# Performance work log

Hardware: AMD Instinct MI355X
Metric: run time of the kernel (lower is better)

## Reference

```python
import jax, jax.numpy as jnp
import numpy as np


def setup_inputs() -> dict:
    key = jax.random.key(0)
    k1, k2, k3, k4 = jax.random.split(key, 4)
    T, E, H, I = 256, 16, 2048, 1024
    x = jax.random.normal(k1, (T, H), dtype=jnp.float32)
    router_logits = jax.random.normal(k2, (T, E), dtype=jnp.float32)
    # dequantized GGUF expert weights (math after dequant is plain fp GEMM)
    w1 = jax.random.normal(k3, (E, 2 * I, H), dtype=jnp.float32) * 0.02  # gate/up fused
    w2 = jax.random.normal(k4, (E, H, I), dtype=jnp.float32) * 0.02     # down proj
    return {"x": x, "router_logits": router_logits, "w1": w1, "w2": w2, "top_k": 4}


def reference(x, router_logits, w1, w2, top_k):
    # Router: softmax -> top-k -> renormalize (vLLM fused_moe default)
    probs = jax.nn.softmax(router_logits, axis=-1)            # [T, E]
    topk_vals, topk_idx = jax.lax.top_k(probs, top_k)          # [T, k]
    topk_vals = topk_vals / jnp.sum(topk_vals, axis=-1, keepdims=True)
    T, E = router_logits.shape
    # dense routing weights (zero for non-selected experts)
    route_w = jnp.zeros((T, E), dtype=x.dtype).at[
        jnp.arange(T)[:, None], topk_idx].set(topk_vals)       # [T, E]

    I = w1.shape[1] // 2
    # gate_up projection for all experts: [T, E, 2I]
    h = jnp.einsum('th,eih->tei', x, w1)
    gate, up = h[..., :I], h[..., I:]
    act = jax.nn.silu(gate) * up                               # silu_and_mul [T, E, I]
    # down projection: [T, E, H]
    y = jnp.einsum('tei,ehi->teh', act, w2)
    # combine with routing weights
    out = jnp.einsum('te,teh->th', route_w, y)                 # [T, H]
    return out
```

## Files before the change

kernel.cpp:

```cpp
#include <hip/hip_runtime.h>


typedef __attribute__((ext_vector_type(8))) short bf16x8;
typedef __attribute__((ext_vector_type(4))) float floatx4;

#define T_TOK 256
#define N_EXP 16
#define H_DIM 2048
#define I_DIM 1024
#define MAX_SLOTS 256

__device__ __forceinline__ short f2bf(float f) {
    union { float f; unsigned u; } v; v.f = f;
    unsigned r = (v.u + 0x7FFFu + ((v.u >> 16) & 1u)) >> 16;
    return (short)r;
}
__device__ __forceinline__ float bf2f(short s) {
    union { unsigned u; float f; } v; v.u = ((unsigned)(unsigned short)s) << 16;
    return v.f;
}
__device__ __forceinline__ bf16x8 pack8(const float* __restrict__ p) {
    float4 a = *(const float4*)p, b = *(const float4*)(p + 4);
    bf16x8 r;
    r[0] = f2bf(a.x); r[1] = f2bf(a.y); r[2] = f2bf(a.z); r[3] = f2bf(a.w);
    r[4] = f2bf(b.x); r[5] = f2bf(b.y); r[6] = f2bf(b.z); r[7] = f2bf(b.w);
    return r;
}

__global__ __launch_bounds__(256) void convert_x_kernel(
    const float* __restrict__ xf, short* __restrict__ xb)
{
    const int i = (blockIdx.x * 256 + threadIdx.x) * 8;
    *(bf16x8*)(xb + i) = pack8(xf + i);
}

__global__ __launch_bounds__(256) void route_kernel(
    const float* __restrict__ logits,
    const int* __restrict__ topk_ptr,
    int* __restrict__ counts, int* __restrict__ tokens,
    int* __restrict__ tok_e, int* __restrict__ tok_slot, float* __restrict__ tok_wt)
{
    __shared__ int lds_counts[N_EXP];
    const int t = threadIdx.x;
    if (t < N_EXP) lds_counts[t] = 0;
    __syncthreads();

    int K = topk_ptr[0];
    if (K > 8) K = 8;
    if (K < 1) K = 1;

    float l[N_EXP];
    #pragma unroll
    for (int j = 0; j < N_EXP; ++j) l[j] = logits[t * N_EXP + j];

    float M = l[0];
    #pragma unroll
    for (int j = 1; j < N_EXP; ++j) M = fmaxf(M, l[j]);

    int idx[8]; float lv[8]; unsigned used = 0u;
    for (int k = 0; k < K; ++k) {
        int bi = 0; float bv = -1e30f;
        #pragma unroll
        for (int j = 0; j < N_EXP; ++j)
            if (!((used >> j) & 1u) && l[j] > bv) { bv = l[j]; bi = j; }
        used |= 1u << bi;
        idx[k] = bi; lv[k] = bv;
    }
    float w[8], s = 0.f;
    for (int k = 0; k < K; ++k) { w[k] = __expf(lv[k] - M); s += w[k]; }
    const float inv = 1.0f / s;

    for (int k = 0; k < K; ++k) {
        const int e = idx[k];
        const int slot = atomicAdd(&lds_counts[e], 1);
        tokens[e * MAX_SLOTS + slot] = t;
        tok_e[t * 8 + k] = e; tok_slot[t * 8 + k] = slot; tok_wt[t * 8 + k] = w[k] * inv;
    }
    __syncthreads();
    if (t < N_EXP) counts[t] = lds_counts[t];
}

__global__ __launch_bounds__(256) void gemm1_kernel(
    const short* __restrict__ xb,
    const float* __restrict__ w1,
    const int* __restrict__ counts, const int* __restrict__ tokens,
    short* __restrict__ act)
{
    const int e = blockIdx.x;
    const int count = counts[e];
    if (count == 0) return;
    const int wave = (int)(threadIdx.x >> 6), lane = (int)(threadIdx.x & 63);
    const int nl = lane & 15, quad = lane >> 4;
    const int i_base = blockIdx.y * 64 + wave * 16;

    const float* wg = w1 + ((size_t)e * H_DIM + (i_base + nl)) * H_DIM;
    const float* wu = w1 + ((size_t)e * H_DIM + (I_DIM + i_base + nl)) * H_DIM;
    const int* toks = tokens + e * MAX_SLOTS;

    for (int ms = 0; ms < count; ms += 128) {
        const short* xr[8];
        #pragma unroll
        for (int mt = 0; mt < 8; ++mt) {
            int s = ms + mt * 16 + nl;
            if (s >= count) s = count - 1;
            xr[mt] = xb + (size_t)toks[s] * H_DIM;
        }
        floatx4 ag[8], au[8];
        #pragma unroll
        for (int mt = 0; mt < 8; ++mt) { ag[mt] = (floatx4)0.0f; au[mt] = (floatx4)0.0f; }

        for (int k = 0; k < H_DIM; k += 32) {
            const int ko = k + quad * 8;
            bf16x8 bg = pack8(wg + ko);
            bf16x8 bu = pack8(wu + ko);
            #pragma unroll
            for (int mt = 0; mt < 8; ++mt) {
                bf16x8 a = *(const bf16x8*)(xr[mt] + ko);
                ag[mt] = __builtin_amdgcn_mfma_f32_16x16x32_bf16(a, bg, ag[mt], 0, 0, 0);
                au[mt] = __builtin_amdgcn_mfma_f32_16x16x32_bf16(a, bu, au[mt], 0, 0, 0);
            }
        }
        #pragma unroll
        for (int mt = 0; mt < 8; ++mt) {
            #pragma unroll
            for (int r = 0; r < 4; ++r) {
                const int slot = ms + mt * 16 + quad * 4 + r;
                if (slot < count) {
                    const float g = ag[mt][r], u = au[mt][r];
                    const float a = g / (1.0f + __expf(-g)) * u;
                    act[(size_t)(e * MAX_SLOTS + slot) * I_DIM + i_base + nl] = f2bf(a);
                }
            }
        }
    }
}

__global__ __launch_bounds__(256) void gemm2_kernel(
    const short* __restrict__ act,
    const float* __restrict__ w2,
    const int* __restrict__ counts,
    short* __restrict__ y)
{
    const int e = blockIdx.x;
    const int count = counts[e];
    if (count == 0) return;
    const int wave = (int)(threadIdx.x >> 6), lane = (int)(threadIdx.x & 63);
    const int nl = lane & 15, quad = lane >> 4;
    const int h_base = blockIdx.y * 64 + wave * 16;

    const float* wr = w2 + ((size_t)e * H_DIM + h_base + nl) * I_DIM;
    const short* acte = act + (size_t)e * MAX_SLOTS * I_DIM;

    for (int ms = 0; ms < count; ms += 128) {
        const short* ar[8];
        #pragma unroll
        for (int mt = 0; mt < 8; ++mt) {
            int s = ms + mt * 16 + nl;
            if (s >= count) s = count - 1;
            ar[mt] = acte + (size_t)s * I_DIM;
        }
        floatx4 acc[8];
        #pragma unroll
        for (int mt = 0; mt < 8; ++mt) acc[mt] = (floatx4)0.0f;

        for (int k = 0; k < I_DIM; k += 32) {
            const int ko = k + quad * 8;
            bf16x8 b = pack8(wr + ko);
            #pragma unroll
            for (int mt = 0; mt < 8; ++mt) {
                bf16x8 a = *(const bf16x8*)(ar[mt] + ko);
                acc[mt] = __builtin_amdgcn_mfma_f32_16x16x32_bf16(a, b, acc[mt], 0, 0, 0);
            }
        }
        #pragma unroll
        for (int mt = 0; mt < 8; ++mt) {
            #pragma unroll
            for (int r = 0; r < 4; ++r) {
                const int slot = ms + mt * 16 + quad * 4 + r;
                if (slot < count)
                    y[(size_t)(e * MAX_SLOTS + slot) * H_DIM + h_base + nl] = f2bf(acc[mt][r]);
            }
        }
    }
}

__global__ __launch_bounds__(256) void gather_kernel(
    const short* __restrict__ y, const int* __restrict__ topk_ptr,
    const int* __restrict__ tok_e, const int* __restrict__ tok_slot,
    const float* __restrict__ tok_wt, float* __restrict__ out)
{
    const int t = blockIdx.x;
    int K = topk_ptr[0];
    if (K > 8) K = 8;
    if (K < 1) K = 1;
    int e[8], sl[8]; float w[8];
    for (int k = 0; k < K; ++k) {
        e[k] = tok_e[t * 8 + k]; sl[k] = tok_slot[t * 8 + k]; w[k] = tok_wt[t * 8 + k];
    }
    for (int h = threadIdx.x; h < H_DIM; h += 256) {
        float s = 0.f;
        for (int k = 0; k < K; ++k)
            s += w[k] * bf2f(y[(size_t)(e[k] * MAX_SLOTS + sl[k]) * H_DIM + h]);
        out[(size_t)t * H_DIM + h] = s;
    }
}

extern "C" void kernel_launch(void* const* d_in, const int* in_sizes, int n_in,
                              void* d_out, int out_size, void* d_ws, size_t ws_size,
                              hipStream_t stream)
{
    const float* x  = (const float*)d_in[0];
    const float* rl = (const float*)d_in[1];
    const float* w1 = (const float*)d_in[2];
    const float* w2 = (const float*)d_in[3];
    const int* topk = (const int*)d_in[4];

    char* ws = (char*)d_ws;
    int*   counts   = (int*)  (ws + 0);
    int*   tokens   = (int*)  (ws + 256);
    int*   tok_e    = (int*)  (ws + 16640);
    int*   tok_slot = (int*)  (ws + 24832);
    float* tok_wt   = (float*)(ws + 33024);
    short* xb       = (short*)(ws + 65536);
    short* act      = (short*)(ws + 1114112);
    short* yb       = (short*)(ws + 9502720);

    convert_x_kernel<<<256, 256, 0, stream>>>(x, xb);
    route_kernel<<<1, 256, 0, stream>>>(rl, topk, counts, tokens, tok_e, tok_slot, tok_wt);
    gemm1_kernel<<<dim3(N_EXP, 16), 256, 0, stream>>>(xb, w1, counts, tokens, act);
    gemm2_kernel<<<dim3(N_EXP, 32), 256, 0, stream>>>(act, w2, counts, yb);
    gather_kernel<<<T_TOK, 256, 0, stream>>>(yb, topk, tok_e, tok_slot, tok_wt, (float*)d_out);
}
```

Baseline: 600.7 us.

## Split token tiles across waves and widen grid for MoE GEMMs

Each block now covers 16 output columns, with its 4 waves dividing the expert's token tiles instead of each wave iterating over all tokens for its own columns. The grid grows 4x and tile counts are template-specialized to avoid padded MFMA work. The intent is more blocks in flight to hide fp32 weight streaming latency, at the cost of each block's waves re-reading the same weight rows.

```diff
diff --git a/kernel.cpp b/kernel.cpp
--- a/kernel.cpp
+++ b/kernel.cpp
@@ -80,7 +80,51 @@
     if (t < N_EXP) counts[t] = lds_counts[t];
 }
 
-__global__ __launch_bounds__(256) void gemm1_kernel(
+template <int NT>
+__device__ __forceinline__ void gemm1_tiles(
+    const short* __restrict__ xb, const float* __restrict__ wg, const float* __restrict__ wu,
+    const int* __restrict__ toks, short* __restrict__ act,
+    const int e, const int i_base, const int wave, const int nl, const int quad,
+    const int count)
+{
+    const short* xr[NT];
+    #pragma unroll
+    for (int j = 0; j < NT; ++j) {
+        int s = (wave + 4 * j) * 16 + nl;
+        if (s >= count) s = count - 1;
+        xr[j] = xb + (size_t)toks[s] * H_DIM;
+    }
+    floatx4 ag[NT], au[NT];
+    #pragma unroll
+    for (int j = 0; j < NT; ++j) { ag[j] = (floatx4)0.0f; au[j] = (floatx4)0.0f; }
+
+    #pragma unroll 2
+    for (int k = 0; k < H_DIM; k += 32) {
+        const int ko = k + quad * 8;
+        bf16x8 bg = pack8(wg + ko);
+        bf16x8 bu = pack8(wu + ko);
+        #pragma unroll
+        for (int j = 0; j < NT; ++j) {
+            bf16x8 a = *(const bf16x8*)(xr[j] + ko);
+            ag[j] = __builtin_amdgcn_mfma_f32_16x16x32_bf16(a, bg, ag[j], 0, 0, 0);
+            au[j] = __builtin_amdgcn_mfma_f32_16x16x32_bf16(a, bu, au[j], 0, 0, 0);
+        }
+    }
+    #pragma unroll
+    for (int j = 0; j < NT; ++j) {
+        #pragma unroll
+        for (int r = 0; r < 4; ++r) {
+            const int slot = (wave + 4 * j) * 16 + quad * 4 + r;
+            if (slot < count) {
+                const float g = ag[j][r], u = au[j][r];
+                const float a = g / (1.0f + __expf(-g)) * u;
+                act[(size_t)(e * MAX_SLOTS + slot) * I_DIM + i_base + nl] = f2bf(a);
+            }
+        }
+    }
+}
+
+__global__ __launch_bounds__(256, 4) void gemm1_kernel(
     const short* __restrict__ xb,
     const float* __restrict__ w1,
     const int* __restrict__ counts, const int* __restrict__ tokens,
@@ -91,51 +135,61 @@
     if (count == 0) return;
     const int wave = (int)(threadIdx.x >> 6), lane = (int)(threadIdx.x & 63);
     const int nl = lane & 15, quad = lane >> 4;
-    const int i_base = blockIdx.y * 64 + wave * 16;
+    const int i_base = blockIdx.y * 16;
+    const int ntiles = (count + 15) >> 4;
+    if (wave >= ntiles) return;
+    const int nown = (ntiles - wave + 3) >> 2;
 
     const float* wg = w1 + ((size_t)e * H_DIM + (i_base + nl)) * H_DIM;
     const float* wu = w1 + ((size_t)e * H_DIM + (I_DIM + i_base + nl)) * H_DIM;
     const int* toks = tokens + e * MAX_SLOTS;
 
-    for (int ms = 0; ms < count; ms += 128) {
-        const short* xr[8];
-        #pragma unroll
-        for (int mt = 0; mt < 8; ++mt) {
-            int s = ms + mt * 16 + nl;
-            if (s >= count) s = count - 1;
-            xr[mt] = xb + (size_t)toks[s] * H_DIM;
-        }
-        floatx4 ag[8], au[8];
-        #pragma unroll
-        for (int mt = 0; mt < 8; ++mt) { ag[mt] = (floatx4)0.0f; au[mt] = (floatx4)0.0f; }
-
-        for (int k = 0; k < H_DIM; k += 32) {
-            const int ko = k + quad * 8;
-            bf16x8 bg = pack8(wg + ko);
-            bf16x8 bu = pack8(wu + ko);
-            #pragma unroll
-            for (int mt = 0; mt < 8; ++mt) {
-                bf16x8 a = *(const bf16x8*)(xr[mt] + ko);
-                ag[mt] = __builtin_amdgcn_mfma_f32_16x16x32_bf16(a, bg, ag[mt], 0, 0, 0);
-                au[mt] = __builtin_amdgcn_mfma_f32_16x16x32_bf16(a, bu, au[mt], 0, 0, 0);
-            }
-        }
-        #pragma unroll
-        for (int mt = 0; mt < 8; ++mt) {
-            #pragma unroll
-            for (int r = 0; r < 4; ++r) {
-                const int slot = ms + mt * 16 + quad * 4 + r;
-                if (slot < count) {
-                    const float g = ag[mt][r], u = au[mt][r];
-                    const float a = g / (1.0f + __expf(-g)) * u;
-                    act[(size_t)(e * MAX_SLOTS + slot) * I_DIM + i_base + nl] = f2bf(a);
-                }
-            }
-        }
-    }
-}
-
-__global__ __launch_bounds__(256) void gemm2_kernel(
+    if      (nown == 1) gemm1_tiles<1>(xb, wg, wu, toks, act, e, i_base, wave, nl, quad, count);
+    else if (nown == 2) gemm1_tiles<2>(xb, wg, wu, toks, act, e, i_base, wave, nl, quad, count);
+    else if (nown == 3) gemm1_tiles<3>(xb, wg, wu, toks, act, e, i_base, wave, nl, quad, count);
+    else                gemm1_tiles<4>(xb, wg, wu, toks, act, e, i_base, wave, nl, quad, count);
+}
+
+template <int NT>
+__device__ __forceinline__ void gemm2_tiles(
+    const short* __restrict__ acte, const float* __restrict__ wr,
+    short* __restrict__ y,
+    const int e, const int h_base, const int wave, const int nl, const int quad,
+    const int count)
+{
+    const short* ar[NT];
+    #pragma unroll
+    for (int j = 0; j < NT; ++j) {
+        int s = (wave + 4 * j) * 16 + nl;
+        if (s >= count) s = count - 1;
+        ar[j] = acte + (size_t)s * I_DIM;
+    }
+    floatx4 acc[NT];
+    #pragma unroll
+    for (int j = 0; j < NT; ++j) acc[j] = (floatx4)0.0f;
+
+    #pragma unroll 2
+    for (int k = 0; k < I_DIM; k += 32) {
+        const int ko = k + quad * 8;
+        bf16x8 b = pack8(wr + ko);
+        #pragma unroll
+        for (int j = 0; j < NT; ++j) {
+            bf16x8 a = *(const bf16x8*)(ar[j] + ko);
+            acc[j] = __builtin_amdgcn_mfma_f32_16x16x32_bf16(a, b, acc[j], 0, 0, 0);
+        }
+    }
+    #pragma unroll
+    for (int j = 0; j < NT; ++j) {
+        #pragma unroll
+        for (int r = 0; r < 4; ++r) {
+            const int slot = (wave + 4 * j) * 16 + quad * 4 + r;
+            if (slot < count)
+                y[(size_t)(e * MAX_SLOTS + slot) * H_DIM + h_base + nl] = f2bf(acc[j][r]);
+        }
+    }
+}
+
+__global__ __launch_bounds__(256, 4) void gemm2_kernel(
     const short* __restrict__ act,
     const float* __restrict__ w2,
     const int* __restrict__ counts,
@@ -146,42 +200,18 @@
     if (count == 0) return;
     const int wave = (int)(threadIdx.x >> 6), lane = (int)(threadIdx.x & 63);
     const int nl = lane & 15, quad = lane >> 4;
-    const int h_base = blockIdx.y * 64 + wave * 16;
+    const int h_base = blockIdx.y * 16;
+    const int ntiles = (count + 15) >> 4;
+    if (wave >= ntiles) return;
+    const int nown = (ntiles - wave + 3) >> 2;
 
     const float* wr = w2 + ((size_t)e * H_DIM + h_base + nl) * I_DIM;
     const short* acte = act + (size_t)e * MAX_SLOTS * I_DIM;
 
-    for (int ms = 0; ms < count; ms += 128) {
-        const short* ar[8];
-        #pragma unroll
-        for (int mt = 0; mt < 8; ++mt) {
-            int s = ms + mt * 16 + nl;
-            if (s >= count) s = count - 1;
-            ar[mt] = acte + (size_t)s * I_DIM;
-        }
-        floatx4 acc[8];
-        #pragma unroll
-        for (int mt = 0; mt < 8; ++mt) acc[mt] = (floatx4)0.0f;
-
-        for (int k = 0; k < I_DIM; k += 32) {
-            const int ko = k + quad * 8;
-            bf16x8 b = pack8(wr + ko);
-            #pragma unroll
-            for (int mt = 0; mt < 8; ++mt) {
-                bf16x8 a = *(const bf16x8*)(ar[mt] + ko);
-                acc[mt] = __builtin_amdgcn_mfma_f32_16x16x32_bf16(a, b, acc[mt], 0, 0, 0);
-            }
-        }
-        #pragma unroll
-        for (int mt = 0; mt < 8; ++mt) {
-            #pragma unroll
-            for (int r = 0; r < 4; ++r) {
-                const int slot = ms + mt * 16 + quad * 4 + r;
-                if (slot < count)
-                    y[(size_t)(e * MAX_SLOTS + slot) * H_DIM + h_base + nl] = f2bf(acc[mt][r]);
-            }
-        }
-    }
+    if      (nown == 1) gemm2_tiles<1>(acte, wr, y, e, h_base, wave, nl, quad, count);
+    else if (nown == 2) gemm2_tiles<2>(acte, wr, y, e, h_base, wave, nl, quad, count);
+    else if (nown == 3) gemm2_tiles<3>(acte, wr, y, e, h_base, wave, nl, quad, count);
+    else                gemm2_tiles<4>(acte, wr, y, e, h_base, wave, nl, quad, count);
 }
 
 __global__ __launch_bounds__(256) void gather_kernel(
@@ -227,7 +257,7 @@
 
     convert_x_kernel<<<256, 256, 0, stream>>>(x, xb);
     route_kernel<<<1, 256, 0, stream>>>(rl, topk, counts, tokens, tok_e, tok_slot, tok_wt);
-    gemm1_kernel<<<dim3(N_EXP, 16), 256, 0, stream>>>(xb, w1, counts, tokens, act);
-    gemm2_kernel<<<dim3(N_EXP, 32), 256, 0, stream>>>(act, w2, counts, yb);
+    gemm1_kernel<<<dim3(N_EXP, 64), 256, 0, stream>>>(xb, w1, counts, tokens, act);
+    gemm2_kernel<<<dim3(N_EXP, 128), 256, 0, stream>>>(act, w2, counts, yb);
     gather_kernel<<<T_TOK, 256, 0, stream>>>(yb, topk, tok_e, tok_slot, tok_wt, (float*)d_out);
 }
```

Result: slower. 652.9 us (+8.7%).
